# Performance work log

Hardware: AMD Instinct MI355X
Metric: run time of the kernel (lower is better)

The kernel has to match this reference:

```python
import jax, jax.numpy as jnp
import numpy as np

B, N, S, K = 16, 4096, 1024, 32
DIN, DINC, DOUT = 64, 67, 64
MAX_VALUE = 1e10


def setup_inputs() -> dict:
    key = jax.random.key(0)
    ks = jax.random.split(key, 6)
    x = jax.random.normal(ks[0], (B, N, DIN), dtype=jnp.float32)
    x_complete = jax.random.normal(ks[1], (B, N, DINC), dtype=jnp.float32)
    # neighbor indices in [-1, N); -1 denotes padding (masked out in pooling)
    indexes = jax.random.randint(ks[2], (B, S, K), -1, N, dtype=jnp.int64)
    # first neighbor is the center point and must be valid
    indexes = indexes.at[:, :, 0].set(jnp.abs(indexes[:, :, 0]) % N)
    weight1 = jax.random.normal(ks[3], (DOUT, DINC), dtype=jnp.float32) * 0.05
    weight2 = jax.random.normal(ks[4], (DOUT, DIN), dtype=jnp.float32) * 0.05
    bias = jax.random.normal(ks[5], (DOUT,), dtype=jnp.float32) * 0.05
    return {"x": x, "x_complete": x_complete, "indexes": indexes,
            "weight1": weight1, "weight2": weight2, "bias": bias, "use_x": 1}


def reference(x, x_complete, indexes, weight1, weight2, bias, use_x):
    # pooling_operation = 'max' (hardcoded; string arg in original module)
    Bq, Nq, _ = x.shape
    _, Sq, Kq = indexes.shape
    C = weight1.shape[0]
    # dense linear projections
    xc = jnp.einsum('bnd,cd->bnc', x_complete, weight1) + bias  # (B,N,C)
    xp = jnp.einsum('bnd,cd->bnc', x, weight2)                  # (B,N,C)
    if use_x:
        xc = xc + xp
    # prepend a zero row so index -1 (-> slot 0) gathers zeros
    pad = jnp.concatenate([jnp.zeros((Bq, 1, C), xc.dtype), xc], axis=1)  # (B,N+1,C)
    idx1 = indexes + 1                                          # (B,S,K)
    g = jnp.take_along_axis(pad, idx1.reshape(Bq, Sq * Kq, 1), axis=1)
    g = g.reshape(Bq, Sq, Kq, C)                                # (B,S,K,C)
    if use_x:
        if Nq == Sq:
            g = g - xp[:, :, None, :]
        else:
            xp_pad = jnp.concatenate([jnp.zeros((Bq, 1, C), xp.dtype), xp], axis=1)
            center = jnp.take_along_axis(xp_pad, (indexes[:, :, 0] + 1)[:, :, None], axis=1)  # (B,S,C)
            g = g - center[:, :, None, :]
    # masked max over the neighbor axis: padded slots pushed to -MAX_VALUE
    mask = (idx1 == 0).astype(g.dtype)[..., None]               # (B,S,K,1)
    out = jnp.max(g - MAX_VALUE * mask, axis=2)                 # (B,S,C)
    return out
```

## Files before the change

### kernel.cpp

```cpp
#include <hip/hip_runtime.h>

#define B_    16
#define N_    4096
#define S_    1024
#define K_    32
#define DIN_  64
#define DINC_ 67
#define DOUT_ 64
#define ROWS_ (B_ * N_)
#define NCH   128
#define NTILE 28
#define ASTR  168
#define WLDSB (NTILE * 64 * 16)
#define ALDSB (64 * ASTR * 2)

typedef float f32x4 __attribute__((ext_vector_type(4)));
typedef short s16x8 __attribute__((ext_vector_type(8)));

static __device__ __forceinline__ unsigned short f2bf(float f) {
    unsigned int u = __float_as_uint(f);
    u = (u + 0x7fffu + ((u >> 16) & 1u)) >> 16;
    return (unsigned short)u;
}
static __device__ __forceinline__ float bf2f(unsigned short h) {
    return __uint_as_float((unsigned int)h << 16);
}
static __device__ __forceinline__ unsigned int pack2(float a, float b) {
    return (unsigned int)f2bf(a) | ((unsigned int)f2bf(b) << 16);
}

__global__ __launch_bounds__(256) void proj_kernel(
    const float* __restrict__ x, const float* __restrict__ xcm,
    const float* __restrict__ w1, const float* __restrict__ w2,
    const float* __restrict__ bias, const int* __restrict__ use_x_p,
    unsigned short* __restrict__ cmb)
{
    __shared__ char smem[WLDSB + ALDSB];
    uint4* ldsb          = (uint4*)smem;
    unsigned short* lwb  = (unsigned short*)smem;
    unsigned short* lact = (unsigned short*)(smem + WLDSB);
    unsigned int*  ldsd  = (unsigned int*)lact;

    const int t    = threadIdx.x;
    const int row0 = (blockIdx.x & 7) * (ROWS_ / 8) + (blockIdx.x >> 3) * 64;
    const int ux   = use_x_p[0];

    ldsb[1536 + t] = make_uint4(0u, 0u, 0u, 0u);
    __syncthreads();

#pragma unroll
    for (int it = 0; it < 2; ++it) {
        const int wid = it * 256 + t;
        const int c   = wid >> 3, kc = wid & 7;
        const int s   = kc >> 2,  q  = kc & 3;
        const float4 v0 = *(const float4*)(w2 + c * DIN_ + kc * 8);
        const float4 v1 = *(const float4*)(w2 + c * DIN_ + kc * 8 + 4);
        uint4 pk;
        pk.x = pack2(v0.x, v0.y); pk.y = pack2(v0.z, v0.w);
        pk.z = pack2(v1.x, v1.y); pk.w = pack2(v1.z, v1.w);
        const int lane = q * 16 + (c & 15);
        ldsb[(s * 8 + 4 + (c >> 4)) * 64 + lane] = pk;
        ldsb[(s * 8 + (c >> 4)) * 64 + lane] =
            ux ? pk : make_uint4(0u, 0u, 0u, 0u);
    }

    {
        const float4* w14 = (const float4*)w1;
#pragma unroll
        for (int jj = 0; jj < 5; ++jj) {
            const int idx = jj * 256 + t;
            if (jj < 4 || idx < 1072) {
                const float4 v = w14[idx];
                const float e4[4] = {v.x, v.y, v.z, v.w};
#pragma unroll
                for (int e = 0; e < 4; ++e) {
                    const int ee = 4 * idx + e;
                    const int c  = ee / 67;
                    const int kk = ee - c * 67 + 64;
                    const int s  = kk >> 5;
                    const int q  = (kk >> 3) & 3;
                    const int j  = kk & 7;
                    const int chunk = (16 + (s - 2) * 4 + (c >> 4)) * 64
                                      + q * 16 + (c & 15);
                    lwb[chunk * 8 + j] = f2bf(e4[e]);
                }
            }
        }
    }

    {
        const float4* sx4 = (const float4*)(x + (size_t)row0 * DIN_);
#pragma unroll
        for (int j = 0; j < 4; ++j) {
            const int idx = j * 256 + t;
            const float4 v = sx4[idx];
            const int row = idx >> 4, f4 = idx & 15;
            *(uint2*)(ldsd + row * 84 + f4 * 2) =
                make_uint2(pack2(v.x, v.y), pack2(v.z, v.w));
        }
    }
    {
        const float4* sc4 = (const float4*)(xcm + (size_t)row0 * DINC_);
#pragma unroll
        for (int j = 0; j < 5; ++j) {
            const int idx = j * 256 + t;
            if (j < 4 || idx < 1072) {
                const float4 v = sc4[idx];
                const float e4[4] = {v.x, v.y, v.z, v.w};
#pragma unroll
                for (int e = 0; e < 4; ++e) {
                    const int ee  = 4 * idx + e;
                    const int row = ee / 67;
                    const int d   = ee - row * 67;
                    lact[row * ASTR + 64 + d] = f2bf(e4[e]);
                }
            }
        }
    }
    if (t < 64) lact[t * ASTR + 131] = 0;
    for (int i = t; i < 64 * 14; i += 256) {
        const int row = i / 14, j2 = i - row * 14;
        ldsd[row * 84 + 66 + j2] = 0;
    }
    __syncthreads();

    const int l = t & 63;
    const int w = __builtin_amdgcn_readfirstlane(t >> 6);
    const int q = l >> 4, m = l & 15;

    const unsigned short* arow = lact + (w * 16 + m) * ASTR;
    s16x8 af[5];
#pragma unroll
    for (int s = 0; s < 5; ++s)
        af[s] = *(const s16x8*)(arow + s * 32 + q * 8);

    const s16x8* bfr = (const s16x8*)ldsb;

    f32x4 acc[8];
#pragma unroll
    for (int nt = 0; nt < 8; ++nt) acc[nt] = (f32x4){0.f, 0.f, 0.f, 0.f};

#pragma unroll
    for (int s = 0; s < 2; ++s)
#pragma unroll
        for (int nt = 0; nt < 8; ++nt)
            acc[nt] = __builtin_amdgcn_mfma_f32_16x16x32_bf16(
                bfr[(s * 8 + nt) * 64 + l], af[s], acc[nt], 0, 0, 0);
#pragma unroll
    for (int s = 2; s < 5; ++s)
#pragma unroll
        for (int nt = 0; nt < 4; ++nt)
            acc[nt] = __builtin_amdgcn_mfma_f32_16x16x32_bf16(
                bfr[(16 + (s - 2) * 4 + nt) * 64 + l], af[s], acc[nt], 0, 0, 0);

    const int row_g = row0 + w * 16 + m;
    unsigned short* rowp = cmb + (size_t)row_g * NCH;
    const int chq = q * 4;
#pragma unroll
    for (int nt = 0; nt < 8; ++nt) {
        f32x4 a = acc[nt];
        if (nt < 4) {
            const float4 bv = *(const float4*)(bias + nt * 16 + chq);
            a[0] += bv.x; a[1] += bv.y; a[2] += bv.z; a[3] += bv.w;
        }
        *(uint2*)(rowp + nt * 16 + chq) =
            make_uint2(pack2(a[0], a[1]), pack2(a[2], a[3]));
    }
}

__global__ __launch_bounds__(256) void gather_max_kernel(
    const int* __restrict__ indexes, const unsigned short* __restrict__ cmb,
    const int* __restrict__ use_x_p, float* __restrict__ out)
{
    const int lane = threadIdx.x & 63;
    const int h    = lane >> 5;
    const int ln   = lane & 31;
    const int wv   = __builtin_amdgcn_readfirstlane(threadIdx.x >> 6);
    const int grp  = (blockIdx.x & 7) * 1024 + (blockIdx.x >> 3) * 4 + wv;
    const int pairA = grp * 2;
    const int b     = grp >> 9;
    const int ux    = use_x_p[0];

    const int* iA = indexes + (size_t)pairA * K_;
    const int* iB = iA + K_;
    const char* cb = (const char*)cmb + (size_t)b * N_ * 256;

    const float NEG = -__builtin_inff();
    float m0 = NEG, m1 = NEG;
#pragma unroll
    for (int k = 0; k < K_; ++k) {
        const int ia = iA[k], ib = iB[k];
        const int ik = h ? ib : ia;
        const int iku = ik < 0 ? 0 : ik;
        const unsigned int v = *(const unsigned int*)(cb + ((size_t)iku << 8) + ln * 4);
        const bool inv = ik < 0;
        m0 = fmaxf(m0, inv ? NEG : bf2f((unsigned short)(v & 0xffff)));
        m1 = fmaxf(m1, inv ? NEG : bf2f((unsigned short)(v >> 16)));
    }
    if (ux) {
        const int i0 = h ? iB[0] : iA[0];
        const unsigned int c = *(const unsigned int*)(cb + ((size_t)i0 << 8) + 128 + ln * 4);
        m0 -= bf2f((unsigned short)(c & 0xffff));
        m1 -= bf2f((unsigned short)(c >> 16));
    }
    const int pair = pairA + h;
    *(float2*)(out + (size_t)pair * 64 + ln * 2) = make_float2(m0, m1);
}

__global__ __launch_bounds__(256, 1) void fused_fallback_kernel(
    const float* __restrict__ x, const float* __restrict__ xcm,
    const int* __restrict__ indexes,
    const float* __restrict__ w1, const float* __restrict__ w2,
    const float* __restrict__ bias, const int* __restrict__ use_x_p,
    float* __restrict__ out)
{
    const int lane = threadIdx.x & 63;
    const int pair = (blockIdx.x * blockDim.x + threadIdx.x) >> 6;
    const int b    = pair >> 10;
    const int ux   = use_x_p[0];

    float W1[DINC_];
#pragma unroll
    for (int j = 0; j < DINC_; ++j) W1[j] = w1[lane * DINC_ + j];
    float W2[DIN_];
#pragma unroll
    for (int j = 0; j < DIN_; ++j) W2[j] = w2[lane * DIN_ + j];
    const float bv = bias[lane];

    const int* idxp  = indexes + (size_t)pair * K_;
    const int  myidx = idxp[lane & 31];

    const float NEG = -__builtin_inff();
    float m = NEG;
    for (int k = 0; k < K_; ++k) {
        const int ik = __shfl(myidx, k, 64);
        if (ik < 0) continue;
        const float* xc_row = xcm + ((size_t)b * N_ + ik) * DINC_;
        float a1 = bv;
#pragma unroll
        for (int j = 0; j < DINC_; ++j) a1 += xc_row[j] * W1[j];
        if (ux) {
            const float* x_row = x + ((size_t)b * N_ + ik) * DIN_;
            float a2 = 0.f;
#pragma unroll
            for (int j = 0; j < DIN_; ++j) a2 += x_row[j] * W2[j];
            a1 += a2;
        }
        m = fmaxf(m, a1);
    }
    if (ux) {
        const int i0 = __shfl(myidx, 0, 64);
        const float* x_row = x + ((size_t)b * N_ + i0) * DIN_;
        float a2 = 0.f;
#pragma unroll
        for (int j = 0; j < DIN_; ++j) a2 += x_row[j] * W2[j];
        m -= a2;
    }
    out[(size_t)pair * DOUT_ + lane] = m;
}

extern "C" void kernel_launch(void* const* d_in, const int* in_sizes, int n_in,
                              void* d_out, int out_size, void* d_ws, size_t ws_size,
                              hipStream_t stream)
{
    const float* x    = (const float*)d_in[0];
    const float* xcm  = (const float*)d_in[1];
    const int*   idx  = (const int*)d_in[2];
    const float* w1   = (const float*)d_in[3];
    const float* w2   = (const float*)d_in[4];
    const float* bias = (const float*)d_in[5];
    const int*   ux   = (const int*)d_in[6];
    float* out = (float*)d_out;

    const size_t cmb_bytes = (size_t)ROWS_ * NCH * sizeof(unsigned short);
    const int npairs = B_ * S_;

    if (ws_size >= cmb_bytes) {
        unsigned short* cmb = (unsigned short*)d_ws;
        proj_kernel<<<ROWS_ / 64, 256, 0, stream>>>(x, xcm, w1, w2, bias, ux, cmb);
        gather_max_kernel<<<(npairs / 2) / 4, 256, 0, stream>>>(idx, cmb, ux, out);
    } else {
        fused_fallback_kernel<<<npairs / 4, 256, 0, stream>>>(x, xcm, idx, w1, w2,
                                                              bias, ux, out);
    }
}
```

Baseline: 104.2 us.

## Add per-batch -inf sentinel row and vectorize projection input staging

The projection output buffer gains one extra row per batch, placed at slot 0. Its feature half is bf16 -inf and its center half is zero, so index -1 maps to that row and the gather needs no clamp or mask select. Gather addressing switches to 32-bit offsets. The projection kernel also stages w1 and x_complete into LDS with 8-wide float4 loads and bf16 packing, replacing per-element division-based scatter. The trade-off is a slightly larger workspace and float4 loads from rows with a 67-float stride, which are not 16-byte aligned.

```diff
diff --git a/kernel.cpp b/kernel.cpp
--- a/kernel.cpp
+++ b/kernel.cpp
@@ -9,6 +9,7 @@
 #define DOUT_ 64
 #define ROWS_ (B_ * N_)
 #define NCH   128
+#define NP1   (N_ + 1)
 #define NTILE 28
 #define ASTR  168
 #define WLDSB (NTILE * 64 * 16)
@@ -44,6 +45,14 @@
     const int t    = threadIdx.x;
     const int row0 = (blockIdx.x & 7) * (ROWS_ / 8) + (blockIdx.x >> 3) * 64;
     const int ux   = use_x_p[0];
+    const int bb   = row0 >> 12;
+
+    if ((row0 & (N_ - 1)) == 0 && t < 16) {
+        uint4* sp = (uint4*)(cmb + (size_t)bb * NP1 * NCH);
+        sp[t] = (t < 8)
+            ? make_uint4(0xff80ff80u, 0xff80ff80u, 0xff80ff80u, 0xff80ff80u)
+            : make_uint4(0u, 0u, 0u, 0u);
+    }
 
     ldsb[1536 + t] = make_uint4(0u, 0u, 0u, 0u);
     __syncthreads();
@@ -64,28 +73,29 @@
             ux ? pk : make_uint4(0u, 0u, 0u, 0u);
     }
 
-    {
-        const float4* w14 = (const float4*)w1;
-#pragma unroll
-        for (int jj = 0; jj < 5; ++jj) {
-            const int idx = jj * 256 + t;
-            if (jj < 4 || idx < 1072) {
-                const float4 v = w14[idx];
-                const float e4[4] = {v.x, v.y, v.z, v.w};
-#pragma unroll
-                for (int e = 0; e < 4; ++e) {
-                    const int ee = 4 * idx + e;
-                    const int c  = ee / 67;
-                    const int kk = ee - c * 67 + 64;
-                    const int s  = kk >> 5;
-                    const int q  = (kk >> 3) & 3;
-                    const int j  = kk & 7;
-                    const int chunk = (16 + (s - 2) * 4 + (c >> 4)) * 64
-                                      + q * 16 + (c & 15);
-                    lwb[chunk * 8 + j] = f2bf(e4[e]);
-                }
-            }
-        }
+#pragma unroll
+    for (int it = 0; it < 2; ++it) {
+        const int wid = it * 256 + t;
+        const int t16 = wid >> 6;
+        const int l   = wid & 63;
+        const int q   = l >> 4, m = l & 15;
+        const int c   = (t16 & 3) * 16 + m;
+        const int db  = ((t16 >> 2) << 5) + q * 8;
+        const float* wp = w1 + c * DINC_ + db;
+        const float4 v0 = *(const float4*)(wp);
+        const float4 v1 = *(const float4*)(wp + 4);
+        uint4 pk;
+        pk.x = pack2(v0.x, v0.y); pk.y = pack2(v0.z, v0.w);
+        pk.z = pack2(v1.x, v1.y); pk.w = pack2(v1.z, v1.w);
+        ldsb[(16 + t16) * 64 + l] = pk;
+    }
+    if (t < 64) {
+        const int c     = t;
+        const int chunk = (24 + (t >> 4)) * 64 + (t & 15);
+        const float* wr = w1 + c * DINC_ + 64;
+        lwb[chunk * 8 + 0] = f2bf(wr[0]);
+        lwb[chunk * 8 + 1] = f2bf(wr[1]);
+        lwb[chunk * 8 + 2] = f2bf(wr[2]);
     }
 
     {
@@ -99,25 +109,23 @@
                 make_uint2(pack2(v.x, v.y), pack2(v.z, v.w));
         }
     }
-    {
-        const float4* sc4 = (const float4*)(xcm + (size_t)row0 * DINC_);
-#pragma unroll
-        for (int j = 0; j < 5; ++j) {
-            const int idx = j * 256 + t;
-            if (j < 4 || idx < 1072) {
-                const float4 v = sc4[idx];
-                const float e4[4] = {v.x, v.y, v.z, v.w};
-#pragma unroll
-                for (int e = 0; e < 4; ++e) {
-                    const int ee  = 4 * idx + e;
-                    const int row = ee / 67;
-                    const int d   = ee - row * 67;
-                    lact[row * ASTR + 64 + d] = f2bf(e4[e]);
-                }
-            }
-        }
-    }
-    if (t < 64) lact[t * ASTR + 131] = 0;
+#pragma unroll
+    for (int it = 0; it < 2; ++it) {
+        const int wid = it * 256 + t;
+        const int row = wid >> 3, dg = wid & 7;
+        const float* sp = xcm + (size_t)(row0 + row) * DINC_ + dg * 8;
+        const float4 v0 = *(const float4*)(sp);
+        const float4 v1 = *(const float4*)(sp + 4);
+        uint4 pk;
+        pk.x = pack2(v0.x, v0.y); pk.y = pack2(v0.z, v0.w);
+        pk.z = pack2(v1.x, v1.y); pk.w = pack2(v1.z, v1.w);
+        *(uint4*)(lact + row * ASTR + 64 + dg * 8) = pk;
+    }
+    if (t < 64) {
+        const float* sp = xcm + (size_t)(row0 + t) * DINC_ + 64;
+        unsigned short* dp = lact + t * ASTR + 128;
+        dp[0] = f2bf(sp[0]); dp[1] = f2bf(sp[1]); dp[2] = f2bf(sp[2]); dp[3] = 0;
+    }
     for (int i = t; i < 64 * 14; i += 256) {
         const int row = i / 14, j2 = i - row * 14;
         ldsd[row * 84 + 66 + j2] = 0;
@@ -154,7 +162,7 @@
                 bfr[(16 + (s - 2) * 4 + nt) * 64 + l], af[s], acc[nt], 0, 0, 0);
 
     const int row_g = row0 + w * 16 + m;
-    unsigned short* rowp = cmb + (size_t)row_g * NCH;
+    unsigned short* rowp = cmb + (size_t)(row_g + bb + 1) * NCH;
     const int chq = q * 4;
 #pragma unroll
     for (int nt = 0; nt < 8; ++nt) {
@@ -183,23 +191,23 @@
 
     const int* iA = indexes + (size_t)pairA * K_;
     const int* iB = iA + K_;
-    const char* cb = (const char*)cmb + (size_t)b * N_ * 256;
+    const char* cb = (const char*)cmb + (size_t)b * NP1 * 256;
+    const unsigned lnoff = (unsigned)(ln << 2);
 
     const float NEG = -__builtin_inff();
     float m0 = NEG, m1 = NEG;
 #pragma unroll
     for (int k = 0; k < K_; ++k) {
-        const int ia = iA[k], ib = iB[k];
-        const int ik = h ? ib : ia;
-        const int iku = ik < 0 ? 0 : ik;
-        const unsigned int v = *(const unsigned int*)(cb + ((size_t)iku << 8) + ln * 4);
-        const bool inv = ik < 0;
-        m0 = fmaxf(m0, inv ? NEG : bf2f((unsigned short)(v & 0xffff)));
-        m1 = fmaxf(m1, inv ? NEG : bf2f((unsigned short)(v >> 16)));
+        const int ik = h ? iB[k] : iA[k];
+        const unsigned off = ((unsigned)(ik + 1) << 8) + lnoff;
+        const unsigned int v = *(const unsigned int*)(cb + off);
+        m0 = fmaxf(m0, bf2f((unsigned short)(v & 0xffff)));
+        m1 = fmaxf(m1, bf2f((unsigned short)(v >> 16)));
     }
     if (ux) {
         const int i0 = h ? iB[0] : iA[0];
-        const unsigned int c = *(const unsigned int*)(cb + ((size_t)i0 << 8) + 128 + ln * 4);
+        const unsigned off0 = ((unsigned)(i0 + 1) << 8) + 128u + lnoff;
+        const unsigned int c = *(const unsigned int*)(cb + off0);
         m0 -= bf2f((unsigned short)(c & 0xffff));
         m1 -= bf2f((unsigned short)(c >> 16));
     }
@@ -272,7 +280,8 @@
     const int*   ux   = (const int*)d_in[6];
     float* out = (float*)d_out;
 
-    const size_t cmb_bytes = (size_t)ROWS_ * NCH * sizeof(unsigned short);
+    const size_t cmb_bytes =
+        (size_t)(ROWS_ + B_) * NCH * sizeof(unsigned short);
     const int npairs = B_ * S_;
 
     if (ws_size >= cmb_bytes) {
```

New measurement: 100.5 us. 3.6% less time.
